# Kernel tuning notes

Hardware: AMD Instinct MI355X
Metric: run time of the kernel (lower is better)

The kernel has to match this reference:

```python
import jax, jax.numpy as jnp
import numpy as np

N_HEADS = 16

def setup_inputs() -> dict:
    key = jax.random.key(0)
    qkv = jax.random.normal(key, (4, 3072, 2048), dtype=jnp.float32)
    return {"qkv": qkv}

def reference(qkv) -> jnp.ndarray:
    bs, width, length = qkv.shape
    ch = width // (3 * N_HEADS)
    # [bs*H, 3*ch, T] -> split into q, k, v each [bs*H, ch, T]
    qkv_r = qkv.reshape(bs * N_HEADS, 3 * ch, length)
    q, k, v = qkv_r[:, :ch], qkv_r[:, ch:2 * ch], qkv_r[:, 2 * ch:]
    scale = 1.0 / jnp.sqrt(jnp.sqrt(jnp.float32(ch)))
    # scores: [bs*H, T, T]
    weight = jnp.einsum('bct,bcs->bts', q * scale, k * scale)
    weight = jax.nn.softmax(weight.astype(jnp.float32), axis=-1).astype(weight.dtype)
    a = jnp.einsum('bts,bcs->bct', weight, v)  # [bs*H, ch, T]
    return a.reshape(bs, N_HEADS * ch, length)
```

## Files before the change

kernel.cpp:

```cpp
#include <hip/hip_runtime.h>

namespace {

constexpr int D  = 64;
constexpr int T  = 2048;
constexpr int TQ = 64;
constexpr int NT = T / 64;
constexpr float SCL = 0.125f * 1.44269504088896340736f;

constexpr size_t QP_OFF  = (size_t)64 * 32 * 8192;
constexpr size_t WS_NEED = ((size_t)64 * 32 * 8192 + (size_t)64 * 32 * 4096) * 2;

typedef __bf16 bf16x8 __attribute__((ext_vector_type(8)));
typedef float  f32x4  __attribute__((ext_vector_type(4)));
typedef unsigned short u16x4 __attribute__((ext_vector_type(4)));
typedef unsigned short u16x8 __attribute__((ext_vector_type(8)));
typedef unsigned int   u32x2 __attribute__((ext_vector_type(2)));

__device__ inline unsigned short f2bf(float f) {
    unsigned int u = __builtin_bit_cast(unsigned int, f);
    u += 0x7FFFu + ((u >> 16) & 1u);
    return (unsigned short)(u >> 16);
}

__device__ inline unsigned int pkbf(float a, float b) {
#if __has_builtin(__builtin_amdgcn_cvt_pk_bf16_f32)
    auto r = __builtin_amdgcn_cvt_pk_bf16_f32(a, b);
    static_assert(sizeof(r) == 4, "cvt_pk_bf16 size");
    return __builtin_bit_cast(unsigned int, r);
#else
    return (unsigned int)f2bf(a) | ((unsigned int)f2bf(b) << 16);
#endif
}

__device__ inline int frag_off(int row, int c0) {
    int g = (c0 >> 3) ^ ((row >> 1) & 7);
    return row * 64 + g * 8;
}

__device__ inline void async_cp16(const void* g, void* l) {
    __builtin_amdgcn_global_load_lds(
        (const __attribute__((address_space(1))) unsigned int*)g,
        (__attribute__((address_space(3))) unsigned int*)l, 16, 0, 0);
}

__global__ __launch_bounds__(256)
void prepass(const float* __restrict__ qkv, unsigned short* __restrict__ ws) {
    const int tile = blockIdx.x, h = blockIdx.y, z = blockIdx.z;
    const int tid = threadIdx.x;
    const float* src = qkv + (size_t)h * 3 * D * T + (size_t)z * D * T + tile * 64;
    __shared__ unsigned short L[4096];

    if (z == 2) {
        unsigned short* dst = ws + (size_t)(h * 32 + tile) * 8192 + 4096;
        #pragma unroll
        for (int half = 0; half < 2; half++) {
            int idx = half * 256 + tid;
            int row = idx >> 3, g = idx & 7;
            int gg  = g ^ ((row >> 1) & 7);
            f32x4 a = *(const f32x4*)(src + (size_t)row * T + gg * 8);
            f32x4 b = *(const f32x4*)(src + (size_t)row * T + gg * 8 + 4);
            u16x8 wv = { f2bf(a[0]), f2bf(a[1]), f2bf(a[2]), f2bf(a[3]),
                         f2bf(b[0]), f2bf(b[1]), f2bf(b[2]), f2bf(b[3]) };
            *(u16x8*)(dst + idx * 8) = wv;
        }
    } else {
        const float m = (z == 0) ? SCL : 1.0f;
        const int c0 = (tid >> 4) * 4, s4 = tid & 15;
        float fr[4][4];
        #pragma unroll
        for (int r = 0; r < 4; r++)
            *(f32x4*)fr[r] = *(const f32x4*)(src + (size_t)(c0 + r) * T + s4 * 4);
        #pragma unroll
        for (int j = 0; j < 4; j++) {
            int trow = s4 * 4 + j;
            u16x4 wv = { f2bf(fr[0][j] * m), f2bf(fr[1][j] * m),
                         f2bf(fr[2][j] * m), f2bf(fr[3][j] * m) };
            *(u16x4*)(L + frag_off(trow, c0) + (c0 & 7)) = wv;
        }
        __syncthreads();
        unsigned short* dst = (z == 0)
            ? ws + QP_OFF + (size_t)(h * 32 + tile) * 4096
            : ws + (size_t)(h * 32 + tile) * 8192;
        #pragma unroll
        for (int i = 0; i < 2; i++)
            *(u16x8*)(dst + tid * 16 + i * 8) =
                *(const u16x8*)(L + tid * 16 + i * 8);
    }
}

__global__ __launch_bounds__(256, 6)
void attn_main(const unsigned short* __restrict__ ws, float* __restrict__ out) {
    const int h  = blockIdx.x;
    const int qt = blockIdx.y;
    const int t0 = qt * TQ;
    const int tid  = threadIdx.x;
    const int lane = tid & 63;
    const int w    = tid >> 6;
    const int sh   = w & 1, th = w >> 1;
    const int ln   = lane & 15, q4 = lane >> 4;

    __shared__ unsigned short KV[8192];
    __shared__ unsigned short Ps[4096];

    const unsigned short* qtile = ws + QP_OFF + (size_t)(h * 32 + qt) * 4096;
    bf16x8 bQ[2][2];
    #pragma unroll
    for (int ti = 0; ti < 2; ti++)
        #pragma unroll
        for (int kc = 0; kc < 2; kc++) {
            int t = th * 32 + ti * 16 + ln;
            bQ[ti][kc] = *(const bf16x8*)(qtile + frag_off(t, kc * 32 + q4 * 8));
        }

    const unsigned short* aKp[2][2];
    const unsigned short* aVp[4];
    const unsigned short* bPp[2];
    unsigned int*         pwp[2][2];
    {
        const unsigned short* Kr = &KV[0];
        const unsigned short* Vr = &KV[4096];
        #pragma unroll
        for (int kc = 0; kc < 2; kc++)
            #pragma unroll
            for (int si = 0; si < 2; si++)
                aKp[kc][si] = Kr + frag_off(sh * 32 + si * 16 + ln, kc * 32 + q4 * 8);
        #pragma unroll
        for (int ci = 0; ci < 4; ci++)
            aVp[ci] = Vr + frag_off(ci * 16 + ln, sh * 32 + q4 * 8);
        #pragma unroll
        for (int ti = 0; ti < 2; ti++) {
            bPp[ti] = Ps + frag_off(th * 32 + ti * 16 + ln, sh * 32 + q4 * 8);
            #pragma unroll
            for (int si = 0; si < 2; si++) {
                int t = th * 32 + ti * 16 + ln, c0p = sh * 32 + si * 16 + q4 * 4;
                pwp[si][ti] = (unsigned int*)(Ps + frag_off(t, c0p) + (c0p & 7));
            }
        }
    }
    char* stage = (char*)&KV[0] + w * 4096;
    const char* kvbase = (const char*)ws + (size_t)(h * 32) * 16384
                         + (size_t)w * 4096 + lane * 16;

    f32x4 acc_o[4][2];
    #pragma unroll
    for (int ci = 0; ci < 4; ci++)
        #pragma unroll
        for (int ti = 0; ti < 2; ti++) acc_o[ci][ti] = (f32x4){0.f, 0.f, 0.f, 0.f};
    float l_acc[2] = {0.f, 0.f};

    #pragma unroll 1
    for (int kt = 0; kt < NT; kt++) {
        __syncthreads();
        {
            const char* gsrc = kvbase + (size_t)kt * 16384;
            #pragma unroll
            for (int i = 0; i < 4; i++) async_cp16(gsrc + i * 1024, stage + i * 1024);
        }
        __syncthreads();

        f32x4 acc_s[2][2];
        #pragma unroll
        for (int si = 0; si < 2; si++)
            #pragma unroll
            for (int ti = 0; ti < 2; ti++) acc_s[si][ti] = (f32x4){0.f, 0.f, 0.f, 0.f};
        #pragma unroll
        for (int kc = 0; kc < 2; kc++)
            #pragma unroll
            for (int si = 0; si < 2; si++) {
                bf16x8 aK = *(const bf16x8*)aKp[kc][si];
                #pragma unroll
                for (int ti = 0; ti < 2; ti++)
                    acc_s[si][ti] = __builtin_amdgcn_mfma_f32_16x16x32_bf16(
                        aK, bQ[ti][kc], acc_s[si][ti], 0, 0, 0);
            }

        #pragma unroll
        for (int si = 0; si < 2; si++)
            #pragma unroll
            for (int ti = 0; ti < 2; ti++) {
                float p0 = __builtin_amdgcn_exp2f(acc_s[si][ti][0]);
                float p1 = __builtin_amdgcn_exp2f(acc_s[si][ti][1]);
                float p2 = __builtin_amdgcn_exp2f(acc_s[si][ti][2]);
                float p3 = __builtin_amdgcn_exp2f(acc_s[si][ti][3]);
                l_acc[ti] += (p0 + p1) + (p2 + p3);
                u32x2 pk = { pkbf(p0, p1), pkbf(p2, p3) };
                *(u32x2*)pwp[si][ti] = pk;
            }

        bf16x8 bP0 = *(const bf16x8*)bPp[0];
        bf16x8 bP1 = *(const bf16x8*)bPp[1];
        #pragma unroll
        for (int ci = 0; ci < 4; ci++) {
            bf16x8 aV = *(const bf16x8*)aVp[ci];
            acc_o[ci][0] = __builtin_amdgcn_mfma_f32_16x16x32_bf16(
                aV, bP0, acc_o[ci][0], 0, 0, 0);
            acc_o[ci][1] = __builtin_amdgcn_mfma_f32_16x16x32_bf16(
                aV, bP1, acc_o[ci][1], 0, 0, 0);
        }
    }

    __syncthreads();
    float* mrg = (float*)&KV[0];
    float* lp  = (float*)Ps;
    #pragma unroll
    for (int ti = 0; ti < 2; ti++) {
        float s = l_acc[ti];
        s += __shfl_xor(s, 16, 64);
        s += __shfl_xor(s, 32, 64);
        if (q4 == 0) lp[th * 64 + sh * 32 + ti * 16 + ln] = s;
    }
    if (sh == 0) {
        float* base = mrg + th * 2048;
        #pragma unroll
        for (int ci = 0; ci < 4; ci++)
            #pragma unroll
            for (int ti = 0; ti < 2; ti++)
                *(f32x4*)(base + (ci * 2 + ti) * 256 + lane * 4) = acc_o[ci][ti];
    }
    __syncthreads();
    if (sh == 1) {
        float* base = mrg + th * 2048;
        float linv[2];
        #pragma unroll
        for (int ti = 0; ti < 2; ti++) {
            int tt = ti * 16 + ln;
            linv[ti] = 1.0f / (lp[th * 64 + tt] + lp[th * 64 + 32 + tt]);
        }
        float* ob = out + (size_t)h * D * T + t0 + th * 32;
        #pragma unroll
        for (int ci = 0; ci < 4; ci++)
            #pragma unroll
            for (int ti = 0; ti < 2; ti++) {
                f32x4 part = *(const f32x4*)(base + (ci * 2 + ti) * 256 + lane * 4);
                #pragma unroll
                for (int r = 0; r < 4; r++) {
                    int c = ci * 16 + q4 * 4 + r;
                    ob[(size_t)c * T + ti * 16 + ln] =
                        (acc_o[ci][ti][r] + part[r]) * linv[ti];
                }
            }
    }
}

__device__ inline bf16x8 frag8(const unsigned short* p, int row, int c0) {
    return *(const bf16x8*)(p + frag_off(row, c0));
}

__global__ __launch_bounds__(256)
void attn_fallback(const float* __restrict__ qkv, float* __restrict__ out) {
    const int h     = blockIdx.y;
    const int t0    = blockIdx.x * TQ;
    const int tid   = threadIdx.x;
    const int lane  = tid & 63;
    const int strip = tid >> 6;
    const int ln    = lane & 15;
    const int q4    = lane >> 4;

    __shared__ unsigned short Qs[TQ * D];
    __shared__ unsigned short Ks[64 * D];
    __shared__ unsigned short Vs[D * 64];
    __shared__ unsigned short Pss[TQ * 64];
    __shared__ float l_lds[TQ];

    const float* qb = qkv + (size_t)h * 3 * D * T;
    const float* kb = qb + (size_t)D * T;
    const float* vb = qb + (size_t)(2 * D) * T;
    const int s4 = tid & 15;
    const int c0 = (tid >> 4) * 4;
    {
        float fr[4][4];
        #pragma unroll
        for (int r = 0; r < 4; r++)
            *(f32x4*)fr[r] = *(const f32x4*)(qb + (size_t)(c0 + r) * T + t0 + s4 * 4);
        #pragma unroll
        for (int j = 0; j < 4; j++) {
            int trow = s4 * 4 + j;
            u16x4 wv = { f2bf(fr[0][j]), f2bf(fr[1][j]), f2bf(fr[2][j]), f2bf(fr[3][j]) };
            *(u16x4*)(Qs + frag_off(trow, c0) + (c0 & 7)) = wv;
        }
    }
    __syncthreads();
    const int arow = strip * 16 + ln;
    const int kg   = q4 * 8;
    const bf16x8 aq0 = frag8(Qs, arow, kg);
    const bf16x8 aq1 = frag8(Qs, arow, 32 + kg);
    f32x4 acc_o[4];
    #pragma unroll
    for (int m = 0; m < 4; m++) acc_o[m] = (f32x4){0.f, 0.f, 0.f, 0.f};
    float l_acc[4] = {0.f, 0.f, 0.f, 0.f};
    constexpr float S2 = 0.125f * 1.44269504088896340736f;
    for (int kt = 0; kt < NT; kt++) {
        const int s0 = kt * 64;
        float kr[4][4], vr[4][4];
        #pragma unroll
        for (int r = 0; r < 4; r++)
            *(f32x4*)kr[r] = *(const f32x4*)(kb + (size_t)(c0 + r) * T + s0 + s4 * 4);
        #pragma unroll
        for (int r = 0; r < 4; r++)
            *(f32x4*)vr[r] = *(const f32x4*)(vb + (size_t)(c0 + r) * T + s0 + s4 * 4);
        __syncthreads();
        #pragma unroll
        for (int j = 0; j < 4; j++) {
            int srow = s4 * 4 + j;
            u16x4 wk = { f2bf(kr[0][j]), f2bf(kr[1][j]), f2bf(kr[2][j]), f2bf(kr[3][j]) };
            *(u16x4*)(Ks + frag_off(srow, c0) + (c0 & 7)) = wk;
        }
        #pragma unroll
        for (int r = 0; r < 4; r++) {
            int row = c0 + r, cc = s4 * 4;
            u16x4 wv = { f2bf(vr[r][0]), f2bf(vr[r][1]), f2bf(vr[r][2]), f2bf(vr[r][3]) };
            *(u16x4*)(Vs + frag_off(row, cc) + (cc & 7)) = wv;
        }
        __syncthreads();
        f32x4 accs[4];
        #pragma unroll
        for (int ns = 0; ns < 4; ns++) {
            bf16x8 b0 = frag8(Ks, ns * 16 + ln, kg);
            bf16x8 b1 = frag8(Ks, ns * 16 + ln, 32 + kg);
            f32x4 z = {0.f, 0.f, 0.f, 0.f};
            z = __builtin_amdgcn_mfma_f32_16x16x32_bf16(aq0, b0, z, 0, 0, 0);
            z = __builtin_amdgcn_mfma_f32_16x16x32_bf16(aq1, b1, z, 0, 0, 0);
            accs[ns] = z;
        }
        #pragma unroll
        for (int ns = 0; ns < 4; ns++) {
            int scol = ns * 16 + ln;
            #pragma unroll
            for (int r = 0; r < 4; r++) {
                float p = __builtin_amdgcn_exp2f(accs[ns][r] * S2);
                l_acc[r] += p;
                int trow = strip * 16 + q4 * 4 + r;
                int g = ((scol >> 3) ^ ((trow >> 1) & 7));
                Pss[trow * 64 + g * 8 + (scol & 7)] = f2bf(p);
            }
        }
        bf16x8 bp0 = frag8(Pss, arow, kg);
        bf16x8 bp1 = frag8(Pss, arow, 32 + kg);
        #pragma unroll
        for (int ms = 0; ms < 4; ms++) {
            bf16x8 av0 = frag8(Vs, ms * 16 + ln, kg);
            bf16x8 av1 = frag8(Vs, ms * 16 + ln, 32 + kg);
            acc_o[ms] = __builtin_amdgcn_mfma_f32_16x16x32_bf16(av0, bp0, acc_o[ms], 0, 0, 0);
            acc_o[ms] = __builtin_amdgcn_mfma_f32_16x16x32_bf16(av1, bp1, acc_o[ms], 0, 0, 0);
        }
    }
    #pragma unroll
    for (int r = 0; r < 4; r++) {
        float s = l_acc[r];
        s += __shfl_xor(s, 1, 64);
        s += __shfl_xor(s, 2, 64);
        s += __shfl_xor(s, 4, 64);
        s += __shfl_xor(s, 8, 64);
        if (ln == 0) l_lds[strip * 16 + q4 * 4 + r] = s;
    }
    const float linv = 1.0f / l_lds[strip * 16 + ln];
    const int tg = t0 + strip * 16 + ln;
    float* ob = out + (size_t)h * D * T;
    #pragma unroll
    for (int ms = 0; ms < 4; ms++)
        #pragma unroll
        for (int r = 0; r < 4; r++) {
            int c = ms * 16 + q4 * 4 + r;
            ob[(size_t)c * T + tg] = acc_o[ms][r] * linv;
        }
}

}

extern "C" void kernel_launch(void* const* d_in, const int* in_sizes, int n_in,
                              void* d_out, int out_size, void* d_ws, size_t ws_size,
                              hipStream_t stream) {
    const float* qkv = (const float*)d_in[0];
    float* out = (float*)d_out;
    if (ws_size >= WS_NEED) {
        prepass<<<dim3(32, 64, 3), 256, 0, stream>>>(qkv, (unsigned short*)d_ws);
        attn_main<<<dim3(64, 32), 256, 0, stream>>>((const unsigned short*)d_ws, out);
    } else {
        attn_fallback<<<dim3(32, 64), 256, 0, stream>>>(qkv, out);
    }
}
```

Before: 279.2 us.

## Load K/V MFMA fragments directly from global memory instead of LDS staging

The per-iteration async copy of each K/V tile into shared memory, and the two block-wide barriers around it, are removed. Each wave now reads its K and V bf16 fragments straight from the pre-swizzled workspace in global memory, relying on L1/L2 caching across the 32 query-tile blocks of a head. Shared memory shrinks to the P staging buffer, which each wave writes and reads itself, plus a small buffer for the row sums. The first score MFMA also takes a zero accumulator directly instead of zeroing registers first. The risk is that global-load latency is now exposed inside a non-unrolled loop with no prefetch, in exchange for no barriers and lower LDS use per block.

```diff
diff --git a/kernel.cpp b/kernel.cpp
--- a/kernel.cpp
+++ b/kernel.cpp
@@ -36,12 +36,6 @@
 __device__ inline int frag_off(int row, int c0) {
     int g = (c0 >> 3) ^ ((row >> 1) & 7);
     return row * 64 + g * 8;
-}
-
-__device__ inline void async_cp16(const void* g, void* l) {
-    __builtin_amdgcn_global_load_lds(
-        (const __attribute__((address_space(1))) unsigned int*)g,
-        (__attribute__((address_space(3))) unsigned int*)l, 16, 0, 0);
 }
 
 __global__ __launch_bounds__(256)
@@ -84,8 +78,7 @@
             : ws + (size_t)(h * 32 + tile) * 8192;
         #pragma unroll
         for (int i = 0; i < 2; i++)
-            *(u16x8*)(dst + tid * 16 + i * 8) =
-                *(const u16x8*)(L + tid * 16 + i * 8);
+            *(u16x8*)(dst + tid * 16 + i * 8) = *(const u16x8*)(L + tid * 16 + i * 8);
     }
 }
 
@@ -100,8 +93,9 @@
     const int sh   = w & 1, th = w >> 1;
     const int ln   = lane & 15, q4 = lane >> 4;
 
-    __shared__ unsigned short KV[8192];
-    __shared__ unsigned short Ps[4096];
+    __shared__ float smem[4096];
+    __shared__ float lbuf[128];
+    unsigned short* Ps = (unsigned short*)smem;
 
     const unsigned short* qtile = ws + QP_OFF + (size_t)(h * 32 + qt) * 4096;
     bf16x8 bQ[2][2];
@@ -113,67 +107,57 @@
             bQ[ti][kc] = *(const bf16x8*)(qtile + frag_off(t, kc * 32 + q4 * 8));
         }
 
-    const unsigned short* aKp[2][2];
-    const unsigned short* aVp[4];
+    int offK[2][2], offV[4];
+    #pragma unroll
+    for (int kc = 0; kc < 2; kc++)
+        #pragma unroll
+        for (int si = 0; si < 2; si++)
+            offK[kc][si] = frag_off(sh * 32 + si * 16 + ln, kc * 32 + q4 * 8);
+    #pragma unroll
+    for (int ci = 0; ci < 4; ci++)
+        offV[ci] = 4096 + frag_off(ci * 16 + ln, sh * 32 + q4 * 8);
+
     const unsigned short* bPp[2];
     unsigned int*         pwp[2][2];
-    {
-        const unsigned short* Kr = &KV[0];
-        const unsigned short* Vr = &KV[4096];
-        #pragma unroll
-        for (int kc = 0; kc < 2; kc++)
-            #pragma unroll
-            for (int si = 0; si < 2; si++)
-                aKp[kc][si] = Kr + frag_off(sh * 32 + si * 16 + ln, kc * 32 + q4 * 8);
-        #pragma unroll
-        for (int ci = 0; ci < 4; ci++)
-            aVp[ci] = Vr + frag_off(ci * 16 + ln, sh * 32 + q4 * 8);
-        #pragma unroll
-        for (int ti = 0; ti < 2; ti++) {
-            bPp[ti] = Ps + frag_off(th * 32 + ti * 16 + ln, sh * 32 + q4 * 8);
-            #pragma unroll
-            for (int si = 0; si < 2; si++) {
-                int t = th * 32 + ti * 16 + ln, c0p = sh * 32 + si * 16 + q4 * 4;
-                pwp[si][ti] = (unsigned int*)(Ps + frag_off(t, c0p) + (c0p & 7));
-            }
-        }
-    }
-    char* stage = (char*)&KV[0] + w * 4096;
-    const char* kvbase = (const char*)ws + (size_t)(h * 32) * 16384
-                         + (size_t)w * 4096 + lane * 16;
+    #pragma unroll
+    for (int ti = 0; ti < 2; ti++) {
+        bPp[ti] = Ps + frag_off(th * 32 + ti * 16 + ln, sh * 32 + q4 * 8);
+        #pragma unroll
+        for (int si = 0; si < 2; si++) {
+            int t = th * 32 + ti * 16 + ln, c0p = sh * 32 + si * 16 + q4 * 4;
+            pwp[si][ti] = (unsigned int*)(Ps + frag_off(t, c0p) + (c0p & 7));
+        }
+    }
+
+    const unsigned short* kv = ws + (size_t)(h * 32) * 8192;
+    const f32x4 ZF = {0.f, 0.f, 0.f, 0.f};
 
     f32x4 acc_o[4][2];
     #pragma unroll
     for (int ci = 0; ci < 4; ci++)
         #pragma unroll
-        for (int ti = 0; ti < 2; ti++) acc_o[ci][ti] = (f32x4){0.f, 0.f, 0.f, 0.f};
+        for (int ti = 0; ti < 2; ti++) acc_o[ci][ti] = ZF;
     float l_acc[2] = {0.f, 0.f};
 
     #pragma unroll 1
-    for (int kt = 0; kt < NT; kt++) {
-        __syncthreads();
-        {
-            const char* gsrc = kvbase + (size_t)kt * 16384;
-            #pragma unroll
-            for (int i = 0; i < 4; i++) async_cp16(gsrc + i * 1024, stage + i * 1024);
-        }
-        __syncthreads();
-
+    for (int kt = 0; kt < NT; kt++, kv += 8192) {
         f32x4 acc_s[2][2];
         #pragma unroll
-        for (int si = 0; si < 2; si++)
-            #pragma unroll
-            for (int ti = 0; ti < 2; ti++) acc_s[si][ti] = (f32x4){0.f, 0.f, 0.f, 0.f};
-        #pragma unroll
-        for (int kc = 0; kc < 2; kc++)
-            #pragma unroll
-            for (int si = 0; si < 2; si++) {
-                bf16x8 aK = *(const bf16x8*)aKp[kc][si];
-                #pragma unroll
-                for (int ti = 0; ti < 2; ti++)
-                    acc_s[si][ti] = __builtin_amdgcn_mfma_f32_16x16x32_bf16(
-                        aK, bQ[ti][kc], acc_s[si][ti], 0, 0, 0);
-            }
+        for (int si = 0; si < 2; si++) {
+            bf16x8 aK0 = *(const bf16x8*)(kv + offK[0][si]);
+            #pragma unroll
+            for (int ti = 0; ti < 2; ti++)
+                acc_s[si][ti] = __builtin_amdgcn_mfma_f32_16x16x32_bf16(
+                    aK0, bQ[ti][0], ZF, 0, 0, 0);
+        }
+        #pragma unroll
+        for (int si = 0; si < 2; si++) {
+            bf16x8 aK1 = *(const bf16x8*)(kv + offK[1][si]);
+            #pragma unroll
+            for (int ti = 0; ti < 2; ti++)
+                acc_s[si][ti] = __builtin_amdgcn_mfma_f32_16x16x32_bf16(
+                    aK1, bQ[ti][1], acc_s[si][ti], 0, 0, 0);
+        }
 
         #pragma unroll
         for (int si = 0; si < 2; si++)
@@ -192,7 +176,7 @@
         bf16x8 bP1 = *(const bf16x8*)bPp[1];
         #pragma unroll
         for (int ci = 0; ci < 4; ci++) {
-            bf16x8 aV = *(const bf16x8*)aVp[ci];
+            bf16x8 aV = *(const bf16x8*)(kv + offV[ci]);
             acc_o[ci][0] = __builtin_amdgcn_mfma_f32_16x16x32_bf16(
                 aV, bP0, acc_o[ci][0], 0, 0, 0);
             acc_o[ci][1] = __builtin_amdgcn_mfma_f32_16x16x32_bf16(
@@ -201,8 +185,7 @@
     }
 
     __syncthreads();
-    float* mrg = (float*)&KV[0];
-    float* lp  = (float*)Ps;
+    float* lp = lbuf;
     #pragma unroll
     for (int ti = 0; ti < 2; ti++) {
         float s = l_acc[ti];
@@ -211,7 +194,7 @@
         if (q4 == 0) lp[th * 64 + sh * 32 + ti * 16 + ln] = s;
     }
     if (sh == 0) {
-        float* base = mrg + th * 2048;
+        float* base = smem + th * 2048;
         #pragma unroll
         for (int ci = 0; ci < 4; ci++)
             #pragma unroll
@@ -220,7 +203,7 @@
     }
     __syncthreads();
     if (sh == 1) {
-        float* base = mrg + th * 2048;
+        float* base = smem + th * 2048;
         float linv[2];
         #pragma unroll
         for (int ti = 0; ti < 2; ti++) {
```

After: 340.9 us. 1.22x slower.
